# Kernel optimization log

Hardware: AMD Instinct MI355X
Metric: run time of the kernel (lower is better)

Reference implementation:

```python
import jax, jax.numpy as jnp
import numpy as np

N = 200000    # nodes
DMAX = 32     # max in-degree (padded)
F = 128       # in_feats
H = 128       # lstm hidden == in_feats (use_pp=False)
OUT = 128     # out_feats


def setup_inputs() -> dict:
    key = jax.random.key(0)
    ks = jax.random.split(key, 11)
    u = lambda k, shape, s: jax.random.uniform(k, shape, jnp.float32, -s, s)
    feat = jax.random.normal(ks[0], (N, F), jnp.float32)
    # norms come from sqrt(degree) in the original; keep them positive, O(1)
    in_norm = jax.random.uniform(ks[1], (N,), jnp.float32) + 1.0
    out_norm = jax.random.uniform(ks[2], (N,), jnp.float32) + 1.0
    neighbors = jax.random.randint(ks[3], (N, DMAX), 0, N, jnp.int32)
    degrees = jax.random.randint(ks[4], (N,), 1, DMAX + 1, jnp.int32)
    s_lstm = 1.0 / np.sqrt(H)   # torch LSTM default init scale
    s_lin = 1.0 / np.sqrt(F)    # module's reset_parameters scale
    W_ih = u(ks[5], (4 * H, F), s_lstm)
    W_hh = u(ks[6], (4 * H, H), s_lstm)
    b_ih = u(ks[7], (4 * H,), s_lstm)
    b_hh = u(ks[8], (4 * H,), s_lstm)
    W_lin = u(ks[9], (OUT, F), s_lin)
    b_lin = u(ks[10], (OUT,), s_lin)
    return dict(feat=feat, in_norm=in_norm, out_norm=out_norm,
                W_ih=W_ih, W_hh=W_hh, b_ih=b_ih, b_hh=b_hh,
                W_lin=W_lin, b_lin=b_lin,
                neighbors=neighbors, degrees=degrees)


def reference(feat, in_norm, out_norm, W_ih, W_hh, b_ih, b_hh, W_lin, b_lin,
              neighbors, degrees):
    # graph.nodes['_U'].data['h'] = feat / out_norm
    msg_src = feat / out_norm[:, None]                      # [N, F]
    n, dmax = neighbors.shape
    h_dim = W_hh.shape[1]
    step_mask = jnp.arange(dmax)[None, :] < degrees[:, None]  # [N, DMAX]

    def step(carry, xs):
        h, c = carry
        idx_t, m_t = xs                                      # [N], [N]
        x = msg_src[idx_t]                                   # gather messages [N, F]
        gates = x @ W_ih.T + b_ih + h @ W_hh.T + b_hh        # [N, 4H]
        i, f, g, o = jnp.split(gates, 4, axis=-1)
        i = jax.nn.sigmoid(i)
        f = jax.nn.sigmoid(f)
        o = jax.nn.sigmoid(o)
        g = jnp.tanh(g)
        c_new = f * c + i * g
        h_new = o * jnp.tanh(c_new)
        m = m_t[:, None]
        return (jnp.where(m, h_new, h), jnp.where(m, c_new, c)), None

    init = (jnp.zeros((n, h_dim), feat.dtype), jnp.zeros((n, h_dim), feat.dtype))
    (h_final, _), _ = jax.lax.scan(step, init, (neighbors.T, step_mask.T))
    # feat = linear(h / in_norm)
    return (h_final / in_norm[:, None]) @ W_lin.T + b_lin
```

## Files before the change

### kernel.cpp

```cpp
#include <hip/hip_runtime.h>

#define NN 200000
#define NB 64
#define NWG (NN / NB)

typedef unsigned short u16;
typedef unsigned int u32;
typedef __attribute__((ext_vector_type(8))) short short8;
typedef __attribute__((ext_vector_type(4))) float f32x4;

#define LOG2E 1.4426950408889634f
#define TWOLOG2E 2.8853900817779268f

__device__ __forceinline__ u16 f2bf(float x) {
  u32 u = __float_as_uint(x);
  u += 0x7FFFu + ((u >> 16) & 1u);
  return (u16)(u >> 16);
}

typedef __attribute__((address_space(3))) unsigned int lds_u32_t;
typedef const __attribute__((address_space(1))) unsigned int glb_u32_t;
__device__ __forceinline__ void gload16(const void* g, void* l) {
  __builtin_amdgcn_global_load_lds((glb_u32_t*)g, (lds_u32_t*)l, 16, 0, 0);
}

__device__ __forceinline__ void spin8(const volatile int* p) {
  while (*p < 8) { }
  asm volatile("" ::: "memory");
}

__global__ void k_prep_msg(const float* __restrict__ feat, const float* __restrict__ onorm,
                           u16* __restrict__ msg) {
  int i = blockIdx.x * 256 + threadIdx.x;
  int row = i >> 4, c8 = (i & 15) * 8;
  const float4 a = *(const float4*)(feat + (size_t)row * 128 + c8);
  const float4 b = *(const float4*)(feat + (size_t)row * 128 + c8 + 4);
  float s = 1.0f / onorm[row];
  short8 v = { (short)f2bf(a.x * s), (short)f2bf(a.y * s), (short)f2bf(a.z * s), (short)f2bf(a.w * s),
               (short)f2bf(b.x * s), (short)f2bf(b.y * s), (short)f2bf(b.z * s), (short)f2bf(b.w * s) };
  *(short8*)(msg + (size_t)row * 128 + c8) = v;
}

__global__ void k_prep_w(const float* __restrict__ Wih, const float* __restrict__ Whh,
                         const float* __restrict__ Wlin, const float* __restrict__ bih,
                         const float* __restrict__ bhh, u16* __restrict__ wihb,
                         u16* __restrict__ whhb, u16* __restrict__ wlinb,
                         float* __restrict__ bsum) {
  int i = blockIdx.x * 256 + threadIdx.x;
  if (i < 65536) {
    int gate = i >> 14;
    float s = (gate == 2) ? TWOLOG2E : -LOG2E;
    wihb[i] = f2bf(Wih[i] * s);
  } else if (i < 131072) {
    int j = i - 65536;
    int gate = j >> 14;
    float s = (gate == 2) ? TWOLOG2E : -LOG2E;
    whhb[j] = f2bf(Whh[j] * s);
  } else if (i < 147456) {
    wlinb[i - 131072] = f2bf(Wlin[i - 131072]);
  } else {
    int j = i - 147456;
    float s = ((j >> 7) == 2) ? TWOLOG2E : -LOG2E;
    bsum[j] = (bih[j] + bhh[j]) * s;
  }
}

__global__ void k_hist(const int* __restrict__ degs, int* __restrict__ hist, int n) {
  __shared__ int lh[33];
  if (threadIdx.x < 33) lh[threadIdx.x] = 0;
  __syncthreads();
  int i = blockIdx.x * 256 + threadIdx.x;
  if (i < n) atomicAdd(&lh[degs[i]], 1);
  __syncthreads();
  if (threadIdx.x < 33 && lh[threadIdx.x]) atomicAdd(&hist[threadIdx.x], lh[threadIdx.x]);
}

__global__ void k_scan(const int* __restrict__ hist, int* __restrict__ basep) {
  if (threadIdx.x == 0 && blockIdx.x == 0) {
    int a = 0;
    for (int d = 32; d >= 1; --d) { basep[d] = a; a += hist[d]; }
    basep[0] = a;
  }
}

__global__ void k_scatter(const int* __restrict__ degs, int* __restrict__ basep,
                          int* __restrict__ perm, int n) {
  __shared__ int lh[33], lbase[33], lc[33];
  int t = threadIdx.x;
  if (t < 33) { lh[t] = 0; lc[t] = 0; }
  __syncthreads();
  int i = blockIdx.x * 256 + t;
  int d = (i < n) ? degs[i] : 0;
  if (i < n) atomicAdd(&lh[d], 1);
  __syncthreads();
  if (t < 33 && lh[t]) lbase[t] = atomicAdd(&basep[t], lh[t]);
  __syncthreads();
  if (i < n) { int r = atomicAdd(&lc[d], 1); perm[lbase[d] + r] = i; }
}

__global__ __launch_bounds__(512, 2) void k_main(
    const u16* __restrict__ msg, const u16* __restrict__ wihb,
    const u16* __restrict__ whhb, const u16* __restrict__ wlinb,
    const float* __restrict__ bsum, const float* __restrict__ blin,
    const float* __restrict__ inorm, const int* __restrict__ nbrs,
    const int* __restrict__ degs, const int* __restrict__ perm,
    float* __restrict__ out) {
  __shared__ alignas(16) u16 Xb[3][64 * 128];
  __shared__ alignas(16) u16 Hb[2][64 * 136];
  __shared__ int gidl[64];
  __shared__ int fl[72];

  const int tid = threadIdx.x;
  const int w = tid >> 6;
  const int lane = tid & 63;
  const int l15 = lane & 15;
  const int g4 = lane >> 4;
  const int w16 = w * 16;
  const int gr = tid >> 4;
  const int xc8 = (((tid & 15) ^ (gr & 15)) * 8);
  const int wbase = w * 512;
  const int base = blockIdx.x * NB;
  volatile int* hr = fl;
  volatile int* xr = fl + 36;

  if (tid < NB) gidl[tid] = perm[base + tid];
  if (tid < 72) fl[tid] = (tid == 0) ? 8 : 0;
  {
    u32* hz = (u32*)Hb[1];
#pragma unroll
    for (int s = 0; s < 8; ++s) hz[tid + s * 512] = 0;
    if (tid < 256) hz[tid + 4096] = 0;
  }
  __syncthreads();

  const int gid0 = gidl[gr], gid1 = gidl[gr + 32];
  const int* nb0 = nbrs + (size_t)gid0 * 32;
  const int* nb1 = nbrs + (size_t)gid1 * 32;

  gload16(msg + (size_t)nb0[0] * 128 + xc8, &Xb[0][wbase]);
  gload16(msg + (size_t)nb1[0] * 128 + xc8, &Xb[0][4096 + wbase]);
  gload16(msg + (size_t)nb0[1] * 128 + xc8, &Xb[1][wbase]);
  gload16(msg + (size_t)nb1[1] * 128 + xc8, &Xb[1][4096 + wbase]);
  int ni0 = nb0[2], ni1 = nb1[2];

  short8 fih[4][4], fhh[4][4];
#pragma unroll
  for (int g = 0; g < 4; ++g)
#pragma unroll
    for (int kk = 0; kk < 4; ++kk) {
      size_t o = (size_t)(g * 128 + w16 + l15) * 128 + kk * 32 + g4 * 8;
      fih[g][kk] = *(const short8*)(wihb + o);
      fhh[g][kk] = *(const short8*)(whhb + o);
    }
  float bias[4];
#pragma unroll
  for (int g = 0; g < 4; ++g) bias[g] = bsum[g * 128 + w16 + l15];

  u32 dgp[4];
#pragma unroll
  for (int r = 0; r < 4; ++r) {
    u32 p = 0;
#pragma unroll
    for (int q = 0; q < 4; ++q) p |= ((u32)degs[gidl[r * 16 + g4 * 4 + q]]) << (8 * q);
    dgp[r] = p;
  }
  const int maxdeg = degs[gidl[0]];

  int xsw[4];
#pragma unroll
  for (int kk = 0; kk < 4; ++kk) xsw[kk] = ((kk * 4 + g4) ^ l15) * 8;

  float c[4][4] = {};
  u32 hpk[4][2] = {};

  asm volatile("s_waitcnt vmcnt(0)" ::: "memory");
  if (lane == 0) { atomicAdd((int*)&xr[0], 1); atomicAdd((int*)&xr[1], 1); }

  for (int t = 0; t < maxdeg; ++t) {
    const u16* Xc = &Xb[t % 3][0];
    const u16* Hc = &Hb[(t + 1) & 1][0];
    u16* Hn = &Hb[t & 1][0];

    spin8(&xr[t]);
    f32x4 acc[2][4];
#pragma unroll
    for (int r = 0; r < 2; ++r)
#pragma unroll
      for (int g = 0; g < 4; ++g) acc[r][g] = (f32x4){bias[g], bias[g], bias[g], bias[g]};
    __builtin_amdgcn_s_setprio(1);
#pragma unroll
    for (int rf = 0; rf < 2; ++rf) {
      short8 ax[4];
#pragma unroll
      for (int kk = 0; kk < 4; ++kk)
        ax[kk] = *(const short8*)(&Xc[(rf * 16 + l15) * 128 + xsw[kk]]);
#pragma unroll
      for (int kk = 0; kk < 4; ++kk)
#pragma unroll
        for (int g = 0; g < 4; ++g)
          acc[rf][g] = __builtin_amdgcn_mfma_f32_16x16x32_bf16(ax[kk], fih[g][kk], acc[rf][g], 0, 0, 0);
    }
    __builtin_amdgcn_s_setprio(0);

    spin8(&hr[t]);

    if (t + 2 < maxdeg) {
      gload16(msg + (size_t)ni0 * 128 + xc8, &Xb[(t + 2) % 3][wbase]);
      gload16(msg + (size_t)ni1 * 128 + xc8, &Xb[(t + 2) % 3][4096 + wbase]);
    }
    { int nt = (t + 3) <= 31 ? (t + 3) : 31; ni0 = nb0[nt]; ni1 = nb1[nt]; }

    __builtin_amdgcn_s_setprio(1);
#pragma unroll
    for (int rf = 0; rf < 2; ++rf) {
      short8 ah[4];
#pragma unroll
      for (int kk = 0; kk < 4; ++kk)
        ah[kk] = *(const short8*)(&Hc[(rf * 16 + l15) * 136 + kk * 32 + g4 * 8]);
#pragma unroll
      for (int kk = 0; kk < 4; ++kk)
#pragma unroll
        for (int g = 0; g < 4; ++g)
          acc[rf][g] = __builtin_amdgcn_mfma_f32_16x16x32_bf16(ah[kk], fhh[g][kk], acc[rf][g], 0, 0, 0);
    }
    __builtin_amdgcn_s_setprio(0);
#pragma unroll
    for (int r = 0; r < 2; ++r)
#pragma unroll
      for (int q = 0; q < 4; ++q) {
        float ei = __builtin_amdgcn_exp2f(acc[r][0][q]);
        float ef = __builtin_amdgcn_exp2f(acc[r][1][q]);
        float eg = __builtin_amdgcn_exp2f(acc[r][2][q]);
        float eo = __builtin_amdgcn_exp2f(acc[r][3][q]);
        float fv  = __builtin_amdgcn_rcpf(1.0f + ef);
        float rig = __builtin_amdgcn_rcpf((1.0f + ei) * (1.0f + eg));
        float ig  = (eg - 1.0f) * rig;
        float cn  = fv * c[r][q] + ig;
        float ec  = __builtin_amdgcn_exp2f(cn * TWOLOG2E);
        float rho = __builtin_amdgcn_rcpf((1.0f + eo) * (1.0f + ec));
        float hn  = (ec - 1.0f) * rho;
        bool act = (int)((dgp[r] >> (8 * q)) & 255u) > t;
        c[r][q] = act ? cn : c[r][q];
        u32 word = hpk[r][q >> 1];
        u16 oldv = (u16)(word >> ((q & 1) * 16));
        u16 nh = act ? f2bf(hn) : oldv;
        hpk[r][q >> 1] = (q & 1) ? ((word & 0x0000FFFFu) | ((u32)nh << 16))
                                 : ((word & 0xFFFF0000u) | (u32)nh);
        Hn[(r * 16 + g4 * 4 + q) * 136 + w16 + l15] = nh;
      }

#pragma unroll
    for (int r = 0; r < 2; ++r)
#pragma unroll
      for (int g = 0; g < 4; ++g) acc[r][g] = (f32x4){bias[g], bias[g], bias[g], bias[g]};
    __builtin_amdgcn_s_setprio(1);
#pragma unroll
    for (int rf = 0; rf < 2; ++rf) {
      short8 ax[4];
#pragma unroll
      for (int kk = 0; kk < 4; ++kk)
        ax[kk] = *(const short8*)(&Xc[(32 + rf * 16 + l15) * 128 + xsw[kk]]);
#pragma unroll
      for (int kk = 0; kk < 4; ++kk)
#pragma unroll
        for (int g = 0; g < 4; ++g)
          acc[rf][g] = __builtin_amdgcn_mfma_f32_16x16x32_bf16(ax[kk], fih[g][kk], acc[rf][g], 0, 0, 0);
    }
#pragma unroll
    for (int rf = 0; rf < 2; ++rf) {
      short8 ah[4];
#pragma unroll
      for (int kk = 0; kk < 4; ++kk)
        ah[kk] = *(const short8*)(&Hc[(32 + rf * 16 + l15) * 136 + kk * 32 + g4 * 8]);
#pragma unroll
      for (int kk = 0; kk < 4; ++kk)
#pragma unroll
        for (int g = 0; g < 4; ++g)
          acc[rf][g] = __builtin_amdgcn_mfma_f32_16x16x32_bf16(ah[kk], fhh[g][kk], acc[rf][g], 0, 0, 0);
    }
    __builtin_amdgcn_s_setprio(0);
#pragma unroll
    for (int r = 0; r < 2; ++r) {
      const int rr = 2 + r;
#pragma unroll
      for (int q = 0; q < 4; ++q) {
        float ei = __builtin_amdgcn_exp2f(acc[r][0][q]);
        float ef = __builtin_amdgcn_exp2f(acc[r][1][q]);
        float eg = __builtin_amdgcn_exp2f(acc[r][2][q]);
        float eo = __builtin_amdgcn_exp2f(acc[r][3][q]);
        float fv  = __builtin_amdgcn_rcpf(1.0f + ef);
        float rig = __builtin_amdgcn_rcpf((1.0f + ei) * (1.0f + eg));
        float ig  = (eg - 1.0f) * rig;
        float cn  = fv * c[rr][q] + ig;
        float ec  = __builtin_amdgcn_exp2f(cn * TWOLOG2E);
        float rho = __builtin_amdgcn_rcpf((1.0f + eo) * (1.0f + ec));
        float hn  = (ec - 1.0f) * rho;
        bool act = (int)((dgp[rr] >> (8 * q)) & 255u) > t;
        c[rr][q] = act ? cn : c[rr][q];
        u32 word = hpk[rr][q >> 1];
        u16 oldv = (u16)(word >> ((q & 1) * 16));
        u16 nh = act ? f2bf(hn) : oldv;
        hpk[rr][q >> 1] = (q & 1) ? ((word & 0x0000FFFFu) | ((u32)nh << 16))
                                  : ((word & 0xFFFF0000u) | (u32)nh);
        Hn[((rr) * 16 + g4 * 4 + q) * 136 + w16 + l15] = nh;
      }
    }

    asm volatile("s_waitcnt vmcnt(0) lgkmcnt(0)" ::: "memory");
    if (lane == 0) {
      atomicAdd((int*)&hr[t + 1], 1);
      atomicAdd((int*)&xr[t + 2], 1);
    }
  }

  spin8(&hr[maxdeg]);
  const u16* Hf = &Hb[(maxdeg - 1) & 1][0];

  short8 wl[4];
#pragma unroll
  for (int kk = 0; kk < 4; ++kk)
    wl[kk] = *(const short8*)(wlinb + (size_t)(w16 + l15) * 128 + kk * 32 + g4 * 8);
  f32x4 a2[4] = {};
#pragma unroll
  for (int kk = 0; kk < 4; ++kk)
#pragma unroll
    for (int r = 0; r < 4; ++r) {
      short8 ah = *(const short8*)(&Hf[(r * 16 + l15) * 136 + kk * 32 + g4 * 8]);
      a2[r] = __builtin_amdgcn_mfma_f32_16x16x32_bf16(ah, wl[kk], a2[r], 0, 0, 0);
    }
  float blv = blin[w16 + l15];
#pragma unroll
  for (int r = 0; r < 4; ++r)
#pragma unroll
    for (int q = 0; q < 4; ++q) {
      int nl = r * 16 + g4 * 4 + q;
      int g = gidl[nl];
      out[(size_t)g * 128 + w16 + l15] = a2[r][q] / inorm[g] + blv;
    }
}

extern "C" void kernel_launch(void* const* d_in, const int* in_sizes, int n_in,
                              void* d_out, int out_size, void* d_ws, size_t ws_size,
                              hipStream_t stream) {
  const float* feat    = (const float*)d_in[0];
  const float* in_norm = (const float*)d_in[1];
  const float* out_nrm = (const float*)d_in[2];
  const float* W_ih    = (const float*)d_in[3];
  const float* W_hh    = (const float*)d_in[4];
  const float* b_ih    = (const float*)d_in[5];
  const float* b_hh    = (const float*)d_in[6];
  const float* W_lin   = (const float*)d_in[7];
  const float* b_lin   = (const float*)d_in[8];
  const int* neighbors = (const int*)d_in[9];
  const int* degrees   = (const int*)d_in[10];
  float* out = (float*)d_out;

  char* ws = (char*)d_ws;
  u16* msg    = (u16*)(ws);
  u16* wihb   = (u16*)(ws + 51200000);
  u16* whhb   = (u16*)(ws + 51331072);
  u16* wlinb  = (u16*)(ws + 51462144);
  float* bsum = (float*)(ws + 51494912);
  int* perm   = (int*)(ws + 51496960);
  int* hist   = (int*)(ws + 52296960);
  int* basep  = hist + 64;
  if (ws_size < 52297600) return;

  hipMemsetAsync(hist, 0, 64 * 4, stream);
  k_prep_msg<<<12500, 256, 0, stream>>>(feat, out_nrm, msg);
  k_prep_w<<<578, 256, 0, stream>>>(W_ih, W_hh, W_lin, b_ih, b_hh, wihb, whhb, wlinb, bsum);
  k_hist<<<782, 256, 0, stream>>>(degrees, hist, NN);
  k_scan<<<1, 1, 0, stream>>>(hist, basep);
  k_scatter<<<782, 256, 0, stream>>>(degrees, basep, perm, NN);
  k_main<<<NWG, 512, 0, stream>>>(msg, wihb, whhb, wlinb, bsum, b_lin, in_norm,
                                  neighbors, degrees, perm, out);
}
```

Before: 1.020 ms.

## Split node tile into two halves with independent flags and degree bounds

The 64-node tile is split into two 32-row halves, each with its own X staging buffers, hidden-state ready flags and gather-ready flags. The second half stops at its own maximum degree, so it skips steps beyond that. Finer per-half signalling is meant to let waves start one half's gate math while other waves are still finishing the other half, instead of waiting at one combined barrier per step. The cost is more spin-waits and atomics, extra flag storage, and more complex buffer-parity bookkeeping at the end.

```diff
diff --git a/kernel.cpp b/kernel.cpp
--- a/kernel.cpp
+++ b/kernel.cpp
@@ -105,10 +105,11 @@
     const float* __restrict__ inorm, const int* __restrict__ nbrs,
     const int* __restrict__ degs, const int* __restrict__ perm,
     float* __restrict__ out) {
-  __shared__ alignas(16) u16 Xb[3][64 * 128];
+  __shared__ alignas(16) u16 XA[3][32 * 128];
+  __shared__ alignas(16) u16 XB[3][32 * 128];
   __shared__ alignas(16) u16 Hb[2][64 * 136];
   __shared__ int gidl[64];
-  __shared__ int fl[72];
+  __shared__ int fl[144];
 
   const int tid = threadIdx.x;
   const int w = tid >> 6;
@@ -120,11 +121,14 @@
   const int xc8 = (((tid & 15) ^ (gr & 15)) * 8);
   const int wbase = w * 512;
   const int base = blockIdx.x * NB;
-  volatile int* hr = fl;
-  volatile int* xr = fl + 36;
+  volatile int* hrA = fl;
+  volatile int* hrB = fl + 36;
+  volatile int* xrA = fl + 72;
+  volatile int* xrB = fl + 108;
 
   if (tid < NB) gidl[tid] = perm[base + tid];
-  if (tid < 72) fl[tid] = (tid == 0) ? 8 : 0;
+  if (tid < 144) fl[tid] = 0;
+  if (tid == 0) { fl[0] = 8; fl[36] = 8; }
   {
     u32* hz = (u32*)Hb[1];
 #pragma unroll
@@ -133,15 +137,15 @@
   }
   __syncthreads();
 
-  const int gid0 = gidl[gr], gid1 = gidl[gr + 32];
-  const int* nb0 = nbrs + (size_t)gid0 * 32;
-  const int* nb1 = nbrs + (size_t)gid1 * 32;
-
-  gload16(msg + (size_t)nb0[0] * 128 + xc8, &Xb[0][wbase]);
-  gload16(msg + (size_t)nb1[0] * 128 + xc8, &Xb[0][4096 + wbase]);
-  gload16(msg + (size_t)nb0[1] * 128 + xc8, &Xb[1][wbase]);
-  gload16(msg + (size_t)nb1[1] * 128 + xc8, &Xb[1][4096 + wbase]);
-  int ni0 = nb0[2], ni1 = nb1[2];
+  const int gidA = gidl[gr], gidB = gidl[32 + gr];
+  const int* nbA = nbrs + (size_t)gidA * 32;
+  const int* nbB = nbrs + (size_t)gidB * 32;
+
+  gload16(msg + (size_t)nbA[0] * 128 + xc8, &XA[0][wbase]);
+  gload16(msg + (size_t)nbB[0] * 128 + xc8, &XB[0][wbase]);
+  gload16(msg + (size_t)nbA[1] * 128 + xc8, &XA[1][wbase]);
+  gload16(msg + (size_t)nbB[1] * 128 + xc8, &XB[1][wbase]);
+  int niA = nbA[2], niB = nbB[2];
 
   short8 fih[4][4], fhh[4][4];
 #pragma unroll
@@ -164,7 +168,8 @@
     for (int q = 0; q < 4; ++q) p |= ((u32)degs[gidl[r * 16 + g4 * 4 + q]]) << (8 * q);
     dgp[r] = p;
   }
-  const int maxdeg = degs[gidl[0]];
+  const int maxdegA = degs[gidl[0]];
+  const int maxdegB = degs[gidl[32]];
 
   int xsw[4];
 #pragma unroll
@@ -174,168 +179,190 @@
   u32 hpk[4][2] = {};
 
   asm volatile("s_waitcnt vmcnt(0)" ::: "memory");
-  if (lane == 0) { atomicAdd((int*)&xr[0], 1); atomicAdd((int*)&xr[1], 1); }
-
-  for (int t = 0; t < maxdeg; ++t) {
-    const u16* Xc = &Xb[t % 3][0];
+  if (lane == 0) {
+    atomicAdd((int*)&xrA[0], 1); atomicAdd((int*)&xrA[1], 1);
+    atomicAdd((int*)&xrB[0], 1); atomicAdd((int*)&xrB[1], 1);
+  }
+
+  for (int t = 0; t < maxdegA; ++t) {
+    const int sl = t % 3, s2 = (t + 2) % 3;
     const u16* Hc = &Hb[(t + 1) & 1][0];
     u16* Hn = &Hb[t & 1][0];
 
-    spin8(&xr[t]);
-    f32x4 acc[2][4];
-#pragma unroll
-    for (int r = 0; r < 2; ++r)
-#pragma unroll
-      for (int g = 0; g < 4; ++g) acc[r][g] = (f32x4){bias[g], bias[g], bias[g], bias[g]};
-    __builtin_amdgcn_s_setprio(1);
-#pragma unroll
-    for (int rf = 0; rf < 2; ++rf) {
-      short8 ax[4];
-#pragma unroll
-      for (int kk = 0; kk < 4; ++kk)
-        ax[kk] = *(const short8*)(&Xc[(rf * 16 + l15) * 128 + xsw[kk]]);
-#pragma unroll
-      for (int kk = 0; kk < 4; ++kk)
-#pragma unroll
-        for (int g = 0; g < 4; ++g)
-          acc[rf][g] = __builtin_amdgcn_mfma_f32_16x16x32_bf16(ax[kk], fih[g][kk], acc[rf][g], 0, 0, 0);
-    }
-    __builtin_amdgcn_s_setprio(0);
-
-    spin8(&hr[t]);
-
-    if (t + 2 < maxdeg) {
-      gload16(msg + (size_t)ni0 * 128 + xc8, &Xb[(t + 2) % 3][wbase]);
-      gload16(msg + (size_t)ni1 * 128 + xc8, &Xb[(t + 2) % 3][4096 + wbase]);
-    }
-    { int nt = (t + 3) <= 31 ? (t + 3) : 31; ni0 = nb0[nt]; ni1 = nb1[nt]; }
-
-    __builtin_amdgcn_s_setprio(1);
-#pragma unroll
-    for (int rf = 0; rf < 2; ++rf) {
-      short8 ah[4];
-#pragma unroll
-      for (int kk = 0; kk < 4; ++kk)
-        ah[kk] = *(const short8*)(&Hc[(rf * 16 + l15) * 136 + kk * 32 + g4 * 8]);
-#pragma unroll
-      for (int kk = 0; kk < 4; ++kk)
-#pragma unroll
-        for (int g = 0; g < 4; ++g)
-          acc[rf][g] = __builtin_amdgcn_mfma_f32_16x16x32_bf16(ah[kk], fhh[g][kk], acc[rf][g], 0, 0, 0);
-    }
-    __builtin_amdgcn_s_setprio(0);
-#pragma unroll
-    for (int r = 0; r < 2; ++r)
-#pragma unroll
-      for (int q = 0; q < 4; ++q) {
-        float ei = __builtin_amdgcn_exp2f(acc[r][0][q]);
-        float ef = __builtin_amdgcn_exp2f(acc[r][1][q]);
-        float eg = __builtin_amdgcn_exp2f(acc[r][2][q]);
-        float eo = __builtin_amdgcn_exp2f(acc[r][3][q]);
-        float fv  = __builtin_amdgcn_rcpf(1.0f + ef);
-        float rig = __builtin_amdgcn_rcpf((1.0f + ei) * (1.0f + eg));
-        float ig  = (eg - 1.0f) * rig;
-        float cn  = fv * c[r][q] + ig;
-        float ec  = __builtin_amdgcn_exp2f(cn * TWOLOG2E);
-        float rho = __builtin_amdgcn_rcpf((1.0f + eo) * (1.0f + ec));
-        float hn  = (ec - 1.0f) * rho;
-        bool act = (int)((dgp[r] >> (8 * q)) & 255u) > t;
-        c[r][q] = act ? cn : c[r][q];
-        u32 word = hpk[r][q >> 1];
-        u16 oldv = (u16)(word >> ((q & 1) * 16));
-        u16 nh = act ? f2bf(hn) : oldv;
-        hpk[r][q >> 1] = (q & 1) ? ((word & 0x0000FFFFu) | ((u32)nh << 16))
-                                 : ((word & 0xFFFF0000u) | (u32)nh);
-        Hn[(r * 16 + g4 * 4 + q) * 136 + w16 + l15] = nh;
+    {
+      spin8(&xrA[t]);
+      f32x4 acc[2][4];
+#pragma unroll
+      for (int r = 0; r < 2; ++r)
+#pragma unroll
+        for (int g = 0; g < 4; ++g) acc[r][g] = (f32x4){bias[g], bias[g], bias[g], bias[g]};
+      __builtin_amdgcn_s_setprio(1);
+#pragma unroll
+      for (int rf = 0; rf < 2; ++rf) {
+        short8 ax[4];
+#pragma unroll
+        for (int kk = 0; kk < 4; ++kk)
+          ax[kk] = *(const short8*)(&XA[sl][(rf * 16 + l15) * 128 + xsw[kk]]);
+#pragma unroll
+        for (int kk = 0; kk < 4; ++kk)
+#pragma unroll
+          for (int g = 0; g < 4; ++g)
+            acc[rf][g] = __builtin_amdgcn_mfma_f32_16x16x32_bf16(ax[kk], fih[g][kk], acc[rf][g], 0, 0, 0);
       }
-
-#pragma unroll
-    for (int r = 0; r < 2; ++r)
-#pragma unroll
-      for (int g = 0; g < 4; ++g) acc[r][g] = (f32x4){bias[g], bias[g], bias[g], bias[g]};
-    __builtin_amdgcn_s_setprio(1);
-#pragma unroll
-    for (int rf = 0; rf < 2; ++rf) {
-      short8 ax[4];
-#pragma unroll
-      for (int kk = 0; kk < 4; ++kk)
-        ax[kk] = *(const short8*)(&Xc[(32 + rf * 16 + l15) * 128 + xsw[kk]]);
-#pragma unroll
-      for (int kk = 0; kk < 4; ++kk)
-#pragma unroll
-        for (int g = 0; g < 4; ++g)
-          acc[rf][g] = __builtin_amdgcn_mfma_f32_16x16x32_bf16(ax[kk], fih[g][kk], acc[rf][g], 0, 0, 0);
-    }
-#pragma unroll
-    for (int rf = 0; rf < 2; ++rf) {
-      short8 ah[4];
-#pragma unroll
-      for (int kk = 0; kk < 4; ++kk)
-        ah[kk] = *(const short8*)(&Hc[(32 + rf * 16 + l15) * 136 + kk * 32 + g4 * 8]);
-#pragma unroll
-      for (int kk = 0; kk < 4; ++kk)
-#pragma unroll
-        for (int g = 0; g < 4; ++g)
-          acc[rf][g] = __builtin_amdgcn_mfma_f32_16x16x32_bf16(ah[kk], fhh[g][kk], acc[rf][g], 0, 0, 0);
-    }
-    __builtin_amdgcn_s_setprio(0);
-#pragma unroll
-    for (int r = 0; r < 2; ++r) {
-      const int rr = 2 + r;
-#pragma unroll
-      for (int q = 0; q < 4; ++q) {
-        float ei = __builtin_amdgcn_exp2f(acc[r][0][q]);
-        float ef = __builtin_amdgcn_exp2f(acc[r][1][q]);
-        float eg = __builtin_amdgcn_exp2f(acc[r][2][q]);
-        float eo = __builtin_amdgcn_exp2f(acc[r][3][q]);
-        float fv  = __builtin_amdgcn_rcpf(1.0f + ef);
-        float rig = __builtin_amdgcn_rcpf((1.0f + ei) * (1.0f + eg));
-        float ig  = (eg - 1.0f) * rig;
-        float cn  = fv * c[rr][q] + ig;
-        float ec  = __builtin_amdgcn_exp2f(cn * TWOLOG2E);
-        float rho = __builtin_amdgcn_rcpf((1.0f + eo) * (1.0f + ec));
-        float hn  = (ec - 1.0f) * rho;
-        bool act = (int)((dgp[rr] >> (8 * q)) & 255u) > t;
-        c[rr][q] = act ? cn : c[rr][q];
-        u32 word = hpk[rr][q >> 1];
-        u16 oldv = (u16)(word >> ((q & 1) * 16));
-        u16 nh = act ? f2bf(hn) : oldv;
-        hpk[rr][q >> 1] = (q & 1) ? ((word & 0x0000FFFFu) | ((u32)nh << 16))
-                                  : ((word & 0xFFFF0000u) | (u32)nh);
-        Hn[((rr) * 16 + g4 * 4 + q) * 136 + w16 + l15] = nh;
+      __builtin_amdgcn_s_setprio(0);
+
+      spin8(&hrA[t]);
+      if (t + 2 < maxdegA) gload16(msg + (size_t)niA * 128 + xc8, &XA[s2][wbase]);
+      { int nt = (t + 3) <= 31 ? (t + 3) : 31; niA = nbA[nt]; }
+
+      __builtin_amdgcn_s_setprio(1);
+#pragma unroll
+      for (int rf = 0; rf < 2; ++rf) {
+        short8 ah[4];
+#pragma unroll
+        for (int kk = 0; kk < 4; ++kk)
+          ah[kk] = *(const short8*)(&Hc[(rf * 16 + l15) * 136 + kk * 32 + g4 * 8]);
+#pragma unroll
+        for (int kk = 0; kk < 4; ++kk)
+#pragma unroll
+          for (int g = 0; g < 4; ++g)
+            acc[rf][g] = __builtin_amdgcn_mfma_f32_16x16x32_bf16(ah[kk], fhh[g][kk], acc[rf][g], 0, 0, 0);
       }
-    }
-
-    asm volatile("s_waitcnt vmcnt(0) lgkmcnt(0)" ::: "memory");
+      __builtin_amdgcn_s_setprio(0);
+#pragma unroll
+      for (int r = 0; r < 2; ++r)
+#pragma unroll
+        for (int q = 0; q < 4; ++q) {
+          float ei = __builtin_amdgcn_exp2f(acc[r][0][q]);
+          float ef = __builtin_amdgcn_exp2f(acc[r][1][q]);
+          float eg = __builtin_amdgcn_exp2f(acc[r][2][q]);
+          float eo = __builtin_amdgcn_exp2f(acc[r][3][q]);
+          float fv  = __builtin_amdgcn_rcpf(1.0f + ef);
+          float rig = __builtin_amdgcn_rcpf((1.0f + ei) * (1.0f + eg));
+          float ig  = (eg - 1.0f) * rig;
+          float cn  = fv * c[r][q] + ig;
+          float ec  = __builtin_amdgcn_exp2f(cn * TWOLOG2E);
+          float rho = __builtin_amdgcn_rcpf((1.0f + eo) * (1.0f + ec));
+          float hn  = (ec - 1.0f) * rho;
+          bool act = (int)((dgp[r] >> (8 * q)) & 255u) > t;
+          c[r][q] = act ? cn : c[r][q];
+          u32 word = hpk[r][q >> 1];
+          u16 oldv = (u16)(word >> ((q & 1) * 16));
+          u16 nh = act ? f2bf(hn) : oldv;
+          hpk[r][q >> 1] = (q & 1) ? ((word & 0x0000FFFFu) | ((u32)nh << 16))
+                                   : ((word & 0xFFFF0000u) | (u32)nh);
+          Hn[(r * 16 + g4 * 4 + q) * 136 + w16 + l15] = nh;
+        }
+      asm volatile("s_waitcnt lgkmcnt(0)" ::: "memory");
+      if (lane == 0) atomicAdd((int*)&hrA[t + 1], 1);
+    }
+
+    if (t < maxdegB) {
+      spin8(&xrB[t]);
+      f32x4 acc[2][4];
+#pragma unroll
+      for (int r = 0; r < 2; ++r)
+#pragma unroll
+        for (int g = 0; g < 4; ++g) acc[r][g] = (f32x4){bias[g], bias[g], bias[g], bias[g]};
+      __builtin_amdgcn_s_setprio(1);
+#pragma unroll
+      for (int rf = 0; rf < 2; ++rf) {
+        short8 ax[4];
+#pragma unroll
+        for (int kk = 0; kk < 4; ++kk)
+          ax[kk] = *(const short8*)(&XB[sl][(rf * 16 + l15) * 128 + xsw[kk]]);
+#pragma unroll
+        for (int kk = 0; kk < 4; ++kk)
+#pragma unroll
+          for (int g = 0; g < 4; ++g)
+            acc[rf][g] = __builtin_amdgcn_mfma_f32_16x16x32_bf16(ax[kk], fih[g][kk], acc[rf][g], 0, 0, 0);
+      }
+      __builtin_amdgcn_s_setprio(0);
+
+      spin8(&hrB[t]);
+      if (t + 2 < maxdegB) gload16(msg + (size_t)niB * 128 + xc8, &XB[s2][wbase]);
+      { int nt = (t + 3) <= 31 ? (t + 3) : 31; niB = nbB[nt]; }
+
+      __builtin_amdgcn_s_setprio(1);
+#pragma unroll
+      for (int rf = 0; rf < 2; ++rf) {
+        short8 ah[4];
+#pragma unroll
+        for (int kk = 0; kk < 4; ++kk)
+          ah[kk] = *(const short8*)(&Hc[(32 + rf * 16 + l15) * 136 + kk * 32 + g4 * 8]);
+#pragma unroll
+        for (int kk = 0; kk < 4; ++kk)
+#pragma unroll
+          for (int g = 0; g < 4; ++g)
+            acc[rf][g] = __builtin_amdgcn_mfma_f32_16x16x32_bf16(ah[kk], fhh[g][kk], acc[rf][g], 0, 0, 0);
+      }
+      __builtin_amdgcn_s_setprio(0);
+#pragma unroll
+      for (int r = 0; r < 2; ++r) {
+        const int rr = 2 + r;
+#pragma unroll
+        for (int q = 0; q < 4; ++q) {
+          float ei = __builtin_amdgcn_exp2f(acc[r][0][q]);
+          float ef = __builtin_amdgcn_exp2f(acc[r][1][q]);
+          float eg = __builtin_amdgcn_exp2f(acc[r][2][q]);
+          float eo = __builtin_amdgcn_exp2f(acc[r][3][q]);
+          float fv  = __builtin_amdgcn_rcpf(1.0f + ef);
+          float rig = __builtin_amdgcn_rcpf((1.0f + ei) * (1.0f + eg));
+          float ig  = (eg - 1.0f) * rig;
+          float cn  = fv * c[rr][q] + ig;
+          float ec  = __builtin_amdgcn_exp2f(cn * TWOLOG2E);
+          float rho = __builtin_amdgcn_rcpf((1.0f + eo) * (1.0f + ec));
+          float hn  = (ec - 1.0f) * rho;
+          bool act = (int)((dgp[rr] >> (8 * q)) & 255u) > t;
+          c[rr][q] = act ? cn : c[rr][q];
+          u32 word = hpk[rr][q >> 1];
+          u16 oldv = (u16)(word >> ((q & 1) * 16));
+          u16 nh = act ? f2bf(hn) : oldv;
+          hpk[rr][q >> 1] = (q & 1) ? ((word & 0x0000FFFFu) | ((u32)nh << 16))
+                                    : ((word & 0xFFFF0000u) | (u32)nh);
+          Hn[(rr * 16 + g4 * 4 + q) * 136 + w16 + l15] = nh;
+        }
+      }
+      asm volatile("s_waitcnt lgkmcnt(0)" ::: "memory");
+      if (lane == 0) atomicAdd((int*)&hrB[t + 1], 1);
+    }
+
+    asm volatile("s_waitcnt vmcnt(0)" ::: "memory");
     if (lane == 0) {
-      atomicAdd((int*)&hr[t + 1], 1);
-      atomicAdd((int*)&xr[t + 2], 1);
-    }
-  }
-
-  spin8(&hr[maxdeg]);
-  const u16* Hf = &Hb[(maxdeg - 1) & 1][0];
+      if (t + 2 < maxdegA) atomicAdd((int*)&xrA[t + 2], 1);
+      if (t + 2 < maxdegB) atomicAdd((int*)&xrB[t + 2], 1);
+    }
+  }
+
+  spin8(&hrA[maxdegA]);
+  spin8(&hrB[maxdegB]);
+  const u16* HfA = &Hb[(maxdegA - 1) & 1][0];
+  const u16* HfB = &Hb[(maxdegB - 1) & 1][0];
 
   short8 wl[4];
 #pragma unroll
   for (int kk = 0; kk < 4; ++kk)
     wl[kk] = *(const short8*)(wlinb + (size_t)(w16 + l15) * 128 + kk * 32 + g4 * 8);
-  f32x4 a2[4] = {};
+  f32x4 aA[2] = {}, aB[2] = {};
 #pragma unroll
   for (int kk = 0; kk < 4; ++kk)
 #pragma unroll
-    for (int r = 0; r < 4; ++r) {
-      short8 ah = *(const short8*)(&Hf[(r * 16 + l15) * 136 + kk * 32 + g4 * 8]);
-      a2[r] = __builtin_amdgcn_mfma_f32_16x16x32_bf16(ah, wl[kk], a2[r], 0, 0, 0);
+    for (int r = 0; r < 2; ++r) {
+      short8 hA = *(const short8*)(&HfA[(r * 16 + l15) * 136 + kk * 32 + g4 * 8]);
+      short8 hB = *(const short8*)(&HfB[(32 + r * 16 + l15) * 136 + kk * 32 + g4 * 8]);
+      aA[r] = __builtin_amdgcn_mfma_f32_16x16x32_bf16(hA, wl[kk], aA[r], 0, 0, 0);
+      aB[r] = __builtin_amdgcn_mfma_f32_16x16x32_bf16(hB, wl[kk], aB[r], 0, 0, 0);
     }
   float blv = blin[w16 + l15];
 #pragma unroll
-  for (int r = 0; r < 4; ++r)
+  for (int r = 0; r < 2; ++r)
 #pragma unroll
     for (int q = 0; q < 4; ++q) {
       int nl = r * 16 + g4 * 4 + q;
-      int g = gidl[nl];
-      out[(size_t)g * 128 + w16 + l15] = a2[r][q] / inorm[g] + blv;
+      int gA = gidl[nl];
+      int gB = gidl[32 + nl];
+      out[(size_t)gA * 128 + w16 + l15] = aA[r][q] / inorm[gA] + blv;
+      out[(size_t)gB * 128 + w16 + l15] = aB[r][q] / inorm[gB] + blv;
     }
 }
 
```

Result: slower. 1.153 ms (+13.1%).
